# Kernel optimization log

Measured on AMD Instinct MI355X. Metric: run time of the kernel, lower is better.

Reference implementation:

```python
import jax, jax.numpy as jnp
import numpy as np

N = 50000
E = 800000
IN_DIM = 256
HID = 64
HEADS = 6
OUT_DIM = 32
NEG_SLOPE = 0.2


def gat_conv(x, src, dst, W, att_src, att_dst, bias, heads, ch, n_nodes):
    """PyG GATConv (eval mode): lin proj, per-edge LeakyReLU attention,
    segment softmax over destination neighborhoods, scatter-add aggregate.
    src/dst already include self-loops. Returns [n_nodes, heads, ch]."""
    h = (x @ W).reshape(n_nodes, heads, ch)            # [N,H,C]
    a_src = jnp.sum(h * att_src, axis=-1)              # [N,H]
    a_dst = jnp.sum(h * att_dst, axis=-1)              # [N,H]
    e = jax.nn.leaky_relu(a_src[src] + a_dst[dst], NEG_SLOPE)   # [E,H]
    m = jax.ops.segment_max(e, dst, num_segments=n_nodes)       # [N,H]
    ex = jnp.exp(e - m[dst])                                    # [E,H]
    denom = jax.ops.segment_sum(ex, dst, num_segments=n_nodes)  # [N,H]
    alpha = ex / denom[dst]                                     # [E,H]
    out = jax.ops.segment_sum(h[src] * alpha[:, :, None], dst, num_segments=n_nodes)
    return out + bias.reshape(1, heads, ch)


def setup_inputs() -> dict:
    key = jax.random.key(0)
    ks = jax.random.split(key, 10)
    x = jax.random.normal(ks[0], (N, IN_DIM), dtype=jnp.float32)
    edge_index = jax.random.randint(ks[1], (2, E), 0, N, dtype=jnp.int64)
    s1 = 1.0 / np.sqrt(IN_DIM)
    W1 = jax.random.normal(ks[2], (IN_DIM, HEADS * HID), dtype=jnp.float32) * s1
    att_src1 = jax.random.normal(ks[3], (1, HEADS, HID), dtype=jnp.float32) * 0.1
    att_dst1 = jax.random.normal(ks[4], (1, HEADS, HID), dtype=jnp.float32) * 0.1
    b1 = jnp.zeros((HEADS * HID,), dtype=jnp.float32)
    s2 = 1.0 / np.sqrt(HEADS * HID)
    W2 = jax.random.normal(ks[5], (HEADS * HID, OUT_DIM), dtype=jnp.float32) * s2
    att_src2 = jax.random.normal(ks[6], (1, 1, OUT_DIM), dtype=jnp.float32) * 0.1
    att_dst2 = jax.random.normal(ks[7], (1, 1, OUT_DIM), dtype=jnp.float32) * 0.1
    b2 = jnp.zeros((OUT_DIM,), dtype=jnp.float32)
    return {"x": x, "edge_index": edge_index, "W1": W1, "att_src1": att_src1,
            "att_dst1": att_dst1, "b1": b1, "W2": W2, "att_src2": att_src2,
            "att_dst2": att_dst2, "b2": b2}


def reference(x, edge_index, W1, att_src1, att_dst1, b1, W2, att_src2, att_dst2, b2):
    # PyG GATConv default add_self_loops=True
    loops = jnp.arange(N, dtype=edge_index.dtype)
    src = jnp.concatenate([edge_index[0], loops])
    dst = jnp.concatenate([edge_index[1], loops])
    h1 = gat_conv(x, src, dst, W1, att_src1, att_dst1, b1, HEADS, HID, N)
    h1 = jax.nn.relu(h1.reshape(N, HEADS * HID))  # concat=True, then ReLU; dropout = identity (eval)
    h2 = gat_conv(h1, src, dst, W2, att_src2, att_dst2, b2, 1, OUT_DIM, N)
    return h2.reshape(N, OUT_DIM)  # concat=False with 1 head == mean == squeeze
```

## Files before the change

kernel.cpp:

```cpp
#include <hip/hip_runtime.h>
#include <hip/hip_bf16.h>

#define NN 50000
#define EE 800000
#define IN_DIM 256
#define HID 64
#define HEADS 6
#define D1 384
#define OUT_DIM 32
#define NEG_SLOPE 0.2f
#define CAP 128
#define NBLK 196

typedef unsigned int uint32;
typedef unsigned short ushort_t;
typedef short short8 __attribute__((ext_vector_type(8)));
typedef float f32x4 __attribute__((ext_vector_type(4)));
typedef ushort_t ushort8 __attribute__((ext_vector_type(8)));

__device__ __forceinline__ ushort_t f2bf(float f) {
    uint32 u = __builtin_bit_cast(uint32, f);
    u += 0x7fffu + ((u >> 16) & 1u);
    return (ushort_t)(u >> 16);
}
__device__ __forceinline__ float bf2f(ushort_t s) {
    uint32 u = ((uint32)s) << 16;
    return __builtin_bit_cast(float, u);
}
__device__ __forceinline__ float lo16(uint32 d) { return __builtin_bit_cast(float, d << 16); }
__device__ __forceinline__ float hi16(uint32 d) { return __builtin_bit_cast(float, d & 0xffff0000u); }


__global__ void hist_kernel(const int* __restrict__ dst, int* __restrict__ deg) {
    int i = blockIdx.x * 256 + threadIdx.x;
    if (i < EE) atomicAdd(&deg[dst[i]], 1);
}

__global__ __launch_bounds__(256) void scan1_kernel(const int* __restrict__ deg,
                                                    int* __restrict__ blockSums) {
    int t = threadIdx.x;
    int i = blockIdx.x * 256 + t;
    int v = (i < NN) ? (deg[i] + 1) : 0;
#pragma unroll
    for (int o = 32; o; o >>= 1) v += __shfl_xor(v, o);
    __shared__ int ws[4];
    if ((t & 63) == 0) ws[t >> 6] = v;
    __syncthreads();
    if (t == 0) blockSums[blockIdx.x] = ws[0] + ws[1] + ws[2] + ws[3];
}

__global__ __launch_bounds__(256) void scan2_kernel(const int* __restrict__ blockSums,
                                                    int* __restrict__ blockPrefix,
                                                    int* __restrict__ offsets) {
    int t = threadIdx.x;
    int lane = t & 63, w = t >> 6;
    int v = (t < NBLK) ? blockSums[t] : 0;
    int x = v;
#pragma unroll
    for (int o = 1; o < 64; o <<= 1) {
        int y = __shfl_up(x, o);
        if (lane >= o) x += y;
    }
    __shared__ int ws[4];
    if (lane == 63) ws[w] = x;
    __syncthreads();
    int wpre = 0;
#pragma unroll
    for (int k = 0; k < 4; ++k) if (k < w) wpre += ws[k];
    int incl = x + wpre;
    if (t < NBLK) blockPrefix[t] = incl - v;
    if (t == NBLK - 1) offsets[NN] = incl;
}

__global__ __launch_bounds__(256) void scan3_kernel(const int* __restrict__ deg,
                                                    const int* __restrict__ blockPrefix,
                                                    int* __restrict__ offsets,
                                                    int* __restrict__ cursor) {
    int t = threadIdx.x;
    int i = blockIdx.x * 256 + t;
    int lane = t & 63, w = t >> 6;
    int v = (i < NN) ? (deg[i] + 1) : 0;
    int x = v;
#pragma unroll
    for (int o = 1; o < 64; o <<= 1) {
        int y = __shfl_up(x, o);
        if (lane >= o) x += y;
    }
    __shared__ int ws[4];
    if (lane == 63) ws[w] = x;
    __syncthreads();
    int wpre = 0;
#pragma unroll
    for (int k = 0; k < 4; ++k) if (k < w) wpre += ws[k];
    int excl = x + wpre - v + blockPrefix[blockIdx.x];
    if (i < NN) { offsets[i] = excl; cursor[i] = excl; }
}

__global__ void scatter_kernel(const int* __restrict__ src, const int* __restrict__ dst,
                               int* __restrict__ cursor, int* __restrict__ srcIdx) {
    int i = blockIdx.x * 256 + threadIdx.x;
    if (i >= EE + NN) return;
    int s, d;
    if (i < EE) { s = src[i]; d = dst[i]; }
    else        { s = i - EE; d = s; }
    int pos = atomicAdd(&cursor[d], 1);
    srcIdx[pos] = s;
}


__global__ __launch_bounds__(256) void w1t_kernel(const float* __restrict__ W1,
                                                  ushort_t* __restrict__ W1Tb) {
    __shared__ float tile[32][33];
    int tx = threadIdx.x & 31, ty = threadIdx.x >> 5;
    int n0 = blockIdx.x * 32;
    int k0 = blockIdx.y * 32;
#pragma unroll
    for (int i = 0; i < 4; ++i)
        tile[ty + i * 8][tx] = W1[(k0 + ty + i * 8) * D1 + n0 + tx];
    __syncthreads();
#pragma unroll
    for (int i = 0; i < 4; ++i)
        W1Tb[(n0 + ty + i * 8) * IN_DIM + k0 + tx] = f2bf(tile[tx][ty + i * 8]);
}

__global__ __launch_bounds__(256) void w2t_kernel(const float* __restrict__ W2,
                                                  ushort_t* __restrict__ W2Tb) {
    int idx = blockIdx.x * 256 + threadIdx.x;
    if (idx < D1 * OUT_DIM) {
        int k = idx >> 5, n = idx & 31;
        W2Tb[n * D1 + k] = f2bf(W2[idx]);
    }
}


#define G1_BM 64
#define G1_BK 64

__global__ __launch_bounds__(256) void gemm1_kernel(const float* __restrict__ A,
                                                    const ushort_t* __restrict__ Bt,
                                                    const float* __restrict__ att_src,
                                                    const float* __restrict__ att_dst,
                                                    ushort_t* __restrict__ Cb,
                                                    float* __restrict__ a_src1,
                                                    float* __restrict__ a_dst1) {
    __shared__ __align__(16) ushort_t As[G1_BM][G1_BK];
    __shared__ __align__(16) ushort_t Bs[D1][G1_BK];
    __shared__ float redS[G1_BM][8];
    __shared__ float redD[G1_BM][8];
    int t = threadIdx.x;
    int m0 = blockIdx.x * G1_BM;
    int wid = t >> 6, lane = t & 63;
    int lrow = lane & 15, lk = lane >> 4;
    f32x4 acc[4][6] = {};
    for (int k0 = 0; k0 < IN_DIM; k0 += G1_BK) {
        {
            int r = t >> 3, c = t & 7;
#pragma unroll
            for (int p = 0; p < 2; ++p) {
                int row = p * 32 + r;
                int gr = m0 + row;
                float4 v0 = make_float4(0.f, 0.f, 0.f, 0.f), v1 = v0;
                if (gr < NN) {
                    const float* g = &A[(size_t)gr * IN_DIM + k0 + c * 8];
                    v0 = *reinterpret_cast<const float4*>(g);
                    v1 = *reinterpret_cast<const float4*>(g + 4);
                }
                ushort8 u;
                u[0] = f2bf(v0.x); u[1] = f2bf(v0.y); u[2] = f2bf(v0.z); u[3] = f2bf(v0.w);
                u[4] = f2bf(v1.x); u[5] = f2bf(v1.y); u[6] = f2bf(v1.z); u[7] = f2bf(v1.w);
                *reinterpret_cast<ushort8*>(&As[row][(c ^ (row & 7)) * 8]) = u;
            }
        }
        {
            int r = t >> 3, c = t & 7;
#pragma unroll
            for (int p = 0; p < 12; ++p) {
                int row = p * 32 + r;
                ushort8 u = *reinterpret_cast<const ushort8*>(&Bt[row * IN_DIM + k0 + c * 8]);
                *reinterpret_cast<ushort8*>(&Bs[row][(c ^ (row & 7)) * 8]) = u;
            }
        }
        __syncthreads();
#pragma unroll
        for (int kk = 0; kk < G1_BK; kk += 32) {
            int ckb = (kk >> 3) + lk;
            short8 af[4];
#pragma unroll
            for (int fm = 0; fm < 4; ++fm) {
                int m = fm * 16 + lrow;
                af[fm] = *reinterpret_cast<const short8*>(&As[m][(ckb ^ (m & 7)) * 8]);
            }
#pragma unroll
            for (int fn = 0; fn < 6; ++fn) {
                int n = wid * 96 + fn * 16 + lrow;
                short8 bfv = *reinterpret_cast<const short8*>(&Bs[n][(ckb ^ (n & 7)) * 8]);
#pragma unroll
                for (int fm = 0; fm < 4; ++fm)
                    acc[fm][fn] = __builtin_amdgcn_mfma_f32_16x16x32_bf16(af[fm], bfv, acc[fm][fn], 0, 0, 0);
            }
        }
        __syncthreads();
    }
    float atS[6], atD[6];
#pragma unroll
    for (int fn = 0; fn < 6; ++fn) {
        int col = wid * 96 + fn * 16 + lrow;
        atS[fn] = att_src[col];
        atD[fn] = att_dst[col];
    }
    int split = (wid & 1) ? 2 : 4;
#pragma unroll
    for (int fm = 0; fm < 4; ++fm) {
#pragma unroll
        for (int r = 0; r < 4; ++r) {
            int rowl = fm * 16 + lk * 4 + r;
            int row = m0 + rowl;
            float vsA = 0.f, vsB = 0.f, vdA = 0.f, vdB = 0.f;
#pragma unroll
            for (int fn = 0; fn < 6; ++fn) {
                float v = acc[fm][fn][r];
                if (fn < split) { vsA += v * atS[fn]; vdA += v * atD[fn]; }
                else            { vsB += v * atS[fn]; vdB += v * atD[fn]; }
            }
#pragma unroll
            for (int o = 8; o; o >>= 1) {
                vsA += __shfl_xor(vsA, o); vsB += __shfl_xor(vsB, o);
                vdA += __shfl_xor(vdA, o); vdB += __shfl_xor(vdB, o);
            }
            if (lrow == 0) {
                redS[rowl][wid * 2 + 0] = vsA; redS[rowl][wid * 2 + 1] = vsB;
                redD[rowl][wid * 2 + 0] = vdA; redD[rowl][wid * 2 + 1] = vdB;
            }
            if (row < NN) {
#pragma unroll
                for (int fn = 0; fn < 6; ++fn) {
                    int col = wid * 96 + fn * 16 + lrow;
                    Cb[(size_t)row * D1 + col] = f2bf(acc[fm][fn][r]);
                }
            }
        }
    }
    __syncthreads();
    if (t < G1_BM) {
        int row = m0 + t;
        if (row < NN) {
            float s0 = redS[t][0], s1 = redS[t][1] + redS[t][2], s2 = redS[t][3];
            float s3 = redS[t][4], s4 = redS[t][5] + redS[t][6], s5 = redS[t][7];
            float d0 = redD[t][0], d1 = redD[t][1] + redD[t][2], d2 = redD[t][3];
            float d3 = redD[t][4], d4 = redD[t][5] + redD[t][6], d5 = redD[t][7];
            float* ps = &a_src1[(size_t)row * HEADS];
            float* pd = &a_dst1[(size_t)row * HEADS];
            ps[0] = s0; ps[1] = s1; ps[2] = s2; ps[3] = s3; ps[4] = s4; ps[5] = s5;
            pd[0] = d0; pd[1] = d1; pd[2] = d2; pd[3] = d3; pd[4] = d4; pd[5] = d5;
        }
    }
}


__global__ __launch_bounds__(256, 4) void agg1_kernel(const uint32* __restrict__ H1d,
                                                      const float* __restrict__ a_src,
                                                      const float* __restrict__ a_dst,
                                                      const int* __restrict__ offsets,
                                                      const int* __restrict__ srcIdx,
                                                      const float* __restrict__ b1,
                                                      uint32* __restrict__ out1d) {
    __shared__ float pl[4][HEADS][CAP + 1];
    __shared__ int   sl[4][CAP];
    int w = threadIdx.x >> 6, lane = threadIdx.x & 63;
    int hb = lane >> 5;
    int n = blockIdx.x * 4 + w;
    const float2* asv = (const float2*)a_src;
    float ad[HEADS];
#pragma unroll
    for (int h = 0; h < HEADS; ++h) ad[h] = a_dst[n * HEADS + h];
    float ldn[HEADS] = {0.f, 0.f, 0.f, 0.f, 0.f, 0.f};
    float acc[6] = {0.f, 0.f, 0.f, 0.f, 0.f, 0.f};
    int beg = offsets[n], end = offsets[n + 1];
    for (int cbeg = beg; cbeg < end; cbeg += CAP) {
        int L = end - cbeg; if (L > CAP) L = CAP;
        for (int tI = lane; tI < L; tI += 64) {
            int s = srcIdx[cbeg + tI];
            sl[w][tI] = s;
            float2 e0 = asv[s * 3 + 0];
            float2 e1 = asv[s * 3 + 1];
            float2 e2 = asv[s * 3 + 2];
            float ev[6] = {e0.x, e0.y, e1.x, e1.y, e2.x, e2.y};
#pragma unroll
            for (int h = 0; h < HEADS; ++h) {
                float e = ev[h] + ad[h];
                e = e > 0.f ? e : NEG_SLOPE * e;
                float p = __expf(e);
                pl[w][h][tI] = p;
                ldn[h] += p;
            }
        }
        int j = 0;
        for (; j + 4 <= L; j += 4) {
            int s0 = sl[w][j], s1 = sl[w][j + 1], s2 = sl[w][j + 2], s3 = sl[w][j + 3];
            const uint32* h0 = H1d + (size_t)s0 * 192 + lane;
            const uint32* h1 = H1d + (size_t)s1 * 192 + lane;
            const uint32* h2 = H1d + (size_t)s2 * 192 + lane;
            const uint32* h3 = H1d + (size_t)s3 * 192 + lane;
            uint32 a0 = h0[0], a1 = h0[64], a2 = h0[128];
            uint32 b0 = h1[0], b1v_ = h1[64], b2 = h1[128];
            uint32 c0 = h2[0], c1 = h2[64], c2 = h2[128];
            uint32 d0 = h3[0], d1 = h3[64], d2 = h3[128];
            float p00 = pl[w][hb][j],     p01 = pl[w][2 + hb][j],     p02 = pl[w][4 + hb][j];
            float p10 = pl[w][hb][j + 1], p11 = pl[w][2 + hb][j + 1], p12 = pl[w][4 + hb][j + 1];
            float p20 = pl[w][hb][j + 2], p21 = pl[w][2 + hb][j + 2], p22 = pl[w][4 + hb][j + 2];
            float p30 = pl[w][hb][j + 3], p31 = pl[w][2 + hb][j + 3], p32 = pl[w][4 + hb][j + 3];
            acc[0] += p00 * lo16(a0); acc[1] += p00 * hi16(a0);
            acc[2] += p01 * lo16(a1); acc[3] += p01 * hi16(a1);
            acc[4] += p02 * lo16(a2); acc[5] += p02 * hi16(a2);
            acc[0] += p10 * lo16(b0); acc[1] += p10 * hi16(b0);
            acc[2] += p11 * lo16(b1v_); acc[3] += p11 * hi16(b1v_);
            acc[4] += p12 * lo16(b2); acc[5] += p12 * hi16(b2);
            acc[0] += p20 * lo16(c0); acc[1] += p20 * hi16(c0);
            acc[2] += p21 * lo16(c1); acc[3] += p21 * hi16(c1);
            acc[4] += p22 * lo16(c2); acc[5] += p22 * hi16(c2);
            acc[0] += p30 * lo16(d0); acc[1] += p30 * hi16(d0);
            acc[2] += p31 * lo16(d1); acc[3] += p31 * hi16(d1);
            acc[4] += p32 * lo16(d2); acc[5] += p32 * hi16(d2);
        }
        for (; j < L; ++j) {
            int s0 = sl[w][j];
            const uint32* h0 = H1d + (size_t)s0 * 192 + lane;
            uint32 x0 = h0[0], x1 = h0[64], x2 = h0[128];
            float p0 = pl[w][hb][j], p1 = pl[w][2 + hb][j], p2 = pl[w][4 + hb][j];
            acc[0] += p0 * lo16(x0); acc[1] += p0 * hi16(x0);
            acc[2] += p1 * lo16(x1); acc[3] += p1 * hi16(x1);
            acc[4] += p2 * lo16(x2); acc[5] += p2 * hi16(x2);
        }
    }
#pragma unroll
    for (int h = 0; h < HEADS; ++h) {
#pragma unroll
        for (int o = 32; o; o >>= 1) ldn[h] += __shfl_xor(ldn[h], o);
    }
    float dsel[3];
#pragma unroll
    for (int k = 0; k < 3; ++k) dsel[k] = hb ? ldn[2 * k + 1] : ldn[2 * k];
    const float2* b1v = (const float2*)b1;
#pragma unroll
    for (int k = 0; k < 3; ++k) {
        float2 bb = b1v[k * 64 + lane];
        float v0 = fmaxf(acc[2 * k]     / dsel[k] + bb.x, 0.f);
        float v1 = fmaxf(acc[2 * k + 1] / dsel[k] + bb.y, 0.f);
        out1d[(size_t)n * 192 + k * 64 + lane] = (uint32)f2bf(v0) | ((uint32)f2bf(v1) << 16);
    }
}


#define G2_ROWS 256

__global__ __launch_bounds__(256) void gemm2_kernel(const ushort_t* __restrict__ Xb,
                                                    const ushort_t* __restrict__ W2Tb,
                                                    const float* __restrict__ att_src2,
                                                    const float* __restrict__ att_dst2,
                                                    ushort_t* __restrict__ H2b,
                                                    float* __restrict__ a_src2,
                                                    float* __restrict__ a_dst2) {
    __shared__ __align__(16) ushort_t Ws[OUT_DIM][D1];
    __shared__ __align__(16) ushort_t Xs[G2_ROWS][64];
    int t = threadIdx.x;
    int wid = t >> 6, lane = t & 63;
    int lrow = lane & 15, lk = lane >> 4;
    int m0 = blockIdx.x * G2_ROWS;
#pragma unroll
    for (int p = 0; p < 6; ++p) {
        int chunk = p * 256 + t;
        int nr = chunk / 48, c = chunk % 48;
        ushort8 u = *reinterpret_cast<const ushort8*>(&W2Tb[nr * D1 + c * 8]);
        int span = c >> 3, cc = c & 7;
        *reinterpret_cast<ushort8*>(&Ws[nr][(cc ^ (nr & 7)) * 8 + span * 64]) = u;
    }
    f32x4 acc[4][2] = {};
    for (int kc = 0; kc < 6; ++kc) {
        int k0 = kc * 64;
        {
            int r = t >> 3, c = t & 7;
#pragma unroll
            for (int p = 0; p < 8; ++p) {
                int row = p * 32 + r;
                int gr = m0 + row;
                ushort8 u = {0, 0, 0, 0, 0, 0, 0, 0};
                if (gr < NN) u = *reinterpret_cast<const ushort8*>(&Xb[(size_t)gr * D1 + k0 + c * 8]);
                *reinterpret_cast<ushort8*>(&Xs[row][(c ^ (row & 7)) * 8]) = u;
            }
        }
        __syncthreads();
#pragma unroll
        for (int kk = 0; kk < 64; kk += 32) {
            int ckb = (kk >> 3) + lk;
            short8 af[4];
#pragma unroll
            for (int fm = 0; fm < 4; ++fm) {
                int mm = wid * 64 + fm * 16 + lrow;
                af[fm] = *reinterpret_cast<const short8*>(&Xs[mm][(ckb ^ (mm & 7)) * 8]);
            }
#pragma unroll
            for (int fn = 0; fn < 2; ++fn) {
                int nn2 = fn * 16 + lrow;
                short8 bfv = *reinterpret_cast<const short8*>(&Ws[nn2][(ckb ^ (nn2 & 7)) * 8 + kc * 64]);
#pragma unroll
                for (int fm = 0; fm < 4; ++fm)
                    acc[fm][fn] = __builtin_amdgcn_mfma_f32_16x16x32_bf16(af[fm], bfv, acc[fm][fn], 0, 0, 0);
            }
        }
        __syncthreads();
    }
    float as2a = att_src2[lrow], as2b = att_src2[16 + lrow];
    float ad2a = att_dst2[lrow], ad2b = att_dst2[16 + lrow];
#pragma unroll
    for (int fm = 0; fm < 4; ++fm) {
#pragma unroll
        for (int r = 0; r < 4; ++r) {
            int row = m0 + wid * 64 + fm * 16 + lk * 4 + r;
            float h0 = acc[fm][0][r], h1 = acc[fm][1][r];
            float vs = h0 * as2a + h1 * as2b;
            float vd = h0 * ad2a + h1 * ad2b;
#pragma unroll
            for (int o = 8; o; o >>= 1) {
                vs += __shfl_xor(vs, o);
                vd += __shfl_xor(vd, o);
            }
            if (row < NN) {
                H2b[(size_t)row * OUT_DIM + lrow]      = f2bf(h0);
                H2b[(size_t)row * OUT_DIM + 16 + lrow] = f2bf(h1);
                if (lrow == 0) { a_src2[row] = vs; a_dst2[row] = vd; }
            }
        }
    }
}


__global__ __launch_bounds__(256, 4) void agg2_kernel(const ushort_t* __restrict__ H2b,
                                                      const float* __restrict__ a_src,
                                                      const float* __restrict__ a_dst,
                                                      const int* __restrict__ offsets,
                                                      const int* __restrict__ srcIdx,
                                                      const float* __restrict__ b2,
                                                      float* __restrict__ out) {
    __shared__ float pl[4][CAP];
    __shared__ int   sl[4][CAP];
    int w = threadIdx.x >> 6, lane = threadIdx.x & 63;
    int n = blockIdx.x * 4 + w;
    int q = lane & 15, par = lane >> 4;
    const uint32* H2d = (const uint32*)H2b;
    float ad = a_dst[n];
    float ldn = 0.f, ax = 0.f, ay = 0.f;
    int beg = offsets[n], end = offsets[n + 1];
    for (int cbeg = beg; cbeg < end; cbeg += CAP) {
        int L = end - cbeg; if (L > CAP) L = CAP;
        for (int tI = lane; tI < L; tI += 64) {
            int s = srcIdx[cbeg + tI];
            sl[w][tI] = s;
            float e = a_src[s] + ad;
            e = e > 0.f ? e : NEG_SLOPE * e;
            float p = __expf(e);
            pl[w][tI] = p;
            ldn += p;
        }
        int j = 0;
        for (; j + 8 <= L; j += 8) {
            int s0 = sl[w][j + par], s1 = sl[w][j + 4 + par];
            float p0 = pl[w][j + par], p1 = pl[w][j + 4 + par];
            uint32 d0 = H2d[(size_t)s0 * 16 + q];
            uint32 d1 = H2d[(size_t)s1 * 16 + q];
            ax += p0 * lo16(d0) + p1 * lo16(d1);
            ay += p0 * hi16(d0) + p1 * hi16(d1);
        }
        for (; j < L; j += 4) {
            int jj = j + par;
            if (jj < L) {
                int s = sl[w][jj];
                float p = pl[w][jj];
                uint32 d = H2d[(size_t)s * 16 + q];
                ax += p * lo16(d);
                ay += p * hi16(d);
            }
        }
    }
#pragma unroll
    for (int o = 32; o; o >>= 1) ldn += __shfl_xor(ldn, o);
    ax += __shfl_xor(ax, 16); ax += __shfl_xor(ax, 32);
    ay += __shfl_xor(ay, 16); ay += __shfl_xor(ay, 32);
    if (lane < 16) {
        float2 bb = ((const float2*)b2)[q];
        float2 o;
        o.x = ax / ldn + bb.x;
        o.y = ay / ldn + bb.y;
        ((float2*)out)[(size_t)n * 16 + q] = o;
    }
}


static inline size_t align256(size_t x) { return (x + 255) & ~size_t(255); }

extern "C" void kernel_launch(void* const* d_in, const int* in_sizes, int n_in,
                              void* d_out, int out_size, void* d_ws, size_t ws_size,
                              hipStream_t stream) {
    const float* x        = (const float*)d_in[0];
    const int*   ei       = (const int*)d_in[1];
    const float* W1       = (const float*)d_in[2];
    const float* att_src1 = (const float*)d_in[3];
    const float* att_dst1 = (const float*)d_in[4];
    const float* b1       = (const float*)d_in[5];
    const float* W2       = (const float*)d_in[6];
    const float* att_src2 = (const float*)d_in[7];
    const float* att_dst2 = (const float*)d_in[8];
    const float* b2       = (const float*)d_in[9];
    float* out = (float*)d_out;

    const int* e_src = ei;
    const int* e_dst = ei + EE;

    char* p = (char*)d_ws;
    ushort_t* H1b   = (ushort_t*)p; p += align256(sizeof(ushort_t) * (size_t)NN * D1);
    ushort_t* OUT1b = (ushort_t*)p; p += align256(sizeof(ushort_t) * (size_t)NN * D1);
    ushort_t* H2b   = (ushort_t*)p; p += align256(sizeof(ushort_t) * (size_t)NN * OUT_DIM);
    ushort_t* W1Tb  = (ushort_t*)p; p += align256(sizeof(ushort_t) * D1 * IN_DIM);
    ushort_t* W2Tb  = (ushort_t*)p; p += align256(sizeof(ushort_t) * D1 * OUT_DIM);
    float* AS1  = (float*)p; p += align256(sizeof(float) * NN * HEADS);
    float* AD1  = (float*)p; p += align256(sizeof(float) * NN * HEADS);
    float* AS2  = (float*)p; p += align256(sizeof(float) * NN);
    float* AD2  = (float*)p; p += align256(sizeof(float) * NN);
    int*   DEG  = (int*)p;   p += align256(sizeof(int) * NN);
    int*   OFF  = (int*)p;   p += align256(sizeof(int) * (NN + 1));
    int*   CUR  = (int*)p;   p += align256(sizeof(int) * NN);
    int*   BSUM = (int*)p;   p += align256(sizeof(int) * NBLK);
    int*   BPRE = (int*)p;   p += align256(sizeof(int) * NBLK);
    int*   SIDX = (int*)p;   p += align256(sizeof(int) * (EE + NN));

    hipMemsetAsync(DEG, 0, sizeof(int) * NN, stream);
    w1t_kernel<<<dim3(D1 / 32, IN_DIM / 32), 256, 0, stream>>>(W1, W1Tb);
    w2t_kernel<<<48, 256, 0, stream>>>(W2, W2Tb);
    hist_kernel<<<(EE + 255) / 256, 256, 0, stream>>>(e_dst, DEG);
    scan1_kernel<<<NBLK, 256, 0, stream>>>(DEG, BSUM);
    scan2_kernel<<<1, 256, 0, stream>>>(BSUM, BPRE, OFF);
    scan3_kernel<<<NBLK, 256, 0, stream>>>(DEG, BPRE, OFF, CUR);
    scatter_kernel<<<(EE + NN + 255) / 256, 256, 0, stream>>>(e_src, e_dst, CUR, SIDX);

    gemm1_kernel<<<(NN + G1_BM - 1) / G1_BM, 256, 0, stream>>>(x, W1Tb, att_src1, att_dst1, H1b, AS1, AD1);
    agg1_kernel<<<NN / 4, 256, 0, stream>>>((const uint32*)H1b, AS1, AD1, OFF, SIDX, b1, (uint32*)OUT1b);

    gemm2_kernel<<<(NN + G2_ROWS - 1) / G2_ROWS, 256, 0, stream>>>(OUT1b, W2Tb, att_src2, att_dst2, H2b, AS2, AD2);
    agg2_kernel<<<NN / 4, 256, 0, stream>>>(H2b, AS2, AD2, OFF, SIDX, b2, out);
}
```

Baseline: 328.7 us.

## Stage full A tile in LDS, read W1 fragments from global, nontemporal stores

The first GEMM now loads the whole 64x256 bf16 activation tile into shared memory once, with a single barrier. The transposed W1 fragments are read straight from global memory (where they should stay L2-resident) instead of being staged in LDS each k-step, which removes the per-k-step barriers and the large B shared buffer. That raises occupancy, but the MFMA loop now waits on global-load latency. The aggregation outputs use nontemporal stores so they do not pollute the cache.

```diff
diff --git a/kernel.cpp b/kernel.cpp
--- a/kernel.cpp
+++ b/kernel.cpp
@@ -16,6 +16,7 @@
 typedef unsigned short ushort_t;
 typedef short short8 __attribute__((ext_vector_type(8)));
 typedef float f32x4 __attribute__((ext_vector_type(4)));
+typedef float f32x2 __attribute__((ext_vector_type(2)));
 typedef ushort_t ushort8 __attribute__((ext_vector_type(8)));
 
 __device__ __forceinline__ ushort_t f2bf(float f) {
@@ -134,7 +135,6 @@
 
 
 #define G1_BM 64
-#define G1_BK 64
 
 __global__ __launch_bounds__(256) void gemm1_kernel(const float* __restrict__ A,
                                                     const ushort_t* __restrict__ Bt,
@@ -143,63 +143,50 @@
                                                     ushort_t* __restrict__ Cb,
                                                     float* __restrict__ a_src1,
                                                     float* __restrict__ a_dst1) {
-    __shared__ __align__(16) ushort_t As[G1_BM][G1_BK];
-    __shared__ __align__(16) ushort_t Bs[D1][G1_BK];
+    __shared__ __align__(16) ushort_t As[G1_BM][IN_DIM];
     __shared__ float redS[G1_BM][8];
     __shared__ float redD[G1_BM][8];
     int t = threadIdx.x;
     int m0 = blockIdx.x * G1_BM;
     int wid = t >> 6, lane = t & 63;
     int lrow = lane & 15, lk = lane >> 4;
+    {
+        int r = t >> 2, cq = (t & 3) * 8;
+        int gr = m0 + r;
+#pragma unroll
+        for (int p = 0; p < 8; ++p) {
+            int c = cq + p;
+            float4 v0 = make_float4(0.f, 0.f, 0.f, 0.f), v1 = v0;
+            if (gr < NN) {
+                const float* g = &A[(size_t)gr * IN_DIM + c * 8];
+                v0 = *reinterpret_cast<const float4*>(g);
+                v1 = *reinterpret_cast<const float4*>(g + 4);
+            }
+            ushort8 u;
+            u[0] = f2bf(v0.x); u[1] = f2bf(v0.y); u[2] = f2bf(v0.z); u[3] = f2bf(v0.w);
+            u[4] = f2bf(v1.x); u[5] = f2bf(v1.y); u[6] = f2bf(v1.z); u[7] = f2bf(v1.w);
+            *reinterpret_cast<ushort8*>(&As[r][(c ^ (r & 7)) * 8]) = u;
+        }
+    }
+    __syncthreads();
     f32x4 acc[4][6] = {};
-    for (int k0 = 0; k0 < IN_DIM; k0 += G1_BK) {
-        {
-            int r = t >> 3, c = t & 7;
-#pragma unroll
-            for (int p = 0; p < 2; ++p) {
-                int row = p * 32 + r;
-                int gr = m0 + row;
-                float4 v0 = make_float4(0.f, 0.f, 0.f, 0.f), v1 = v0;
-                if (gr < NN) {
-                    const float* g = &A[(size_t)gr * IN_DIM + k0 + c * 8];
-                    v0 = *reinterpret_cast<const float4*>(g);
-                    v1 = *reinterpret_cast<const float4*>(g + 4);
-                }
-                ushort8 u;
-                u[0] = f2bf(v0.x); u[1] = f2bf(v0.y); u[2] = f2bf(v0.z); u[3] = f2bf(v0.w);
-                u[4] = f2bf(v1.x); u[5] = f2bf(v1.y); u[6] = f2bf(v1.z); u[7] = f2bf(v1.w);
-                *reinterpret_cast<ushort8*>(&As[row][(c ^ (row & 7)) * 8]) = u;
-            }
-        }
-        {
-            int r = t >> 3, c = t & 7;
-#pragma unroll
-            for (int p = 0; p < 12; ++p) {
-                int row = p * 32 + r;
-                ushort8 u = *reinterpret_cast<const ushort8*>(&Bt[row * IN_DIM + k0 + c * 8]);
-                *reinterpret_cast<ushort8*>(&Bs[row][(c ^ (row & 7)) * 8]) = u;
-            }
-        }
-        __syncthreads();
-#pragma unroll
-        for (int kk = 0; kk < G1_BK; kk += 32) {
-            int ckb = (kk >> 3) + lk;
-            short8 af[4];
-#pragma unroll
-            for (int fm = 0; fm < 4; ++fm) {
-                int m = fm * 16 + lrow;
-                af[fm] = *reinterpret_cast<const short8*>(&As[m][(ckb ^ (m & 7)) * 8]);
-            }
-#pragma unroll
-            for (int fn = 0; fn < 6; ++fn) {
-                int n = wid * 96 + fn * 16 + lrow;
-                short8 bfv = *reinterpret_cast<const short8*>(&Bs[n][(ckb ^ (n & 7)) * 8]);
-#pragma unroll
-                for (int fm = 0; fm < 4; ++fm)
-                    acc[fm][fn] = __builtin_amdgcn_mfma_f32_16x16x32_bf16(af[fm], bfv, acc[fm][fn], 0, 0, 0);
-            }
-        }
-        __syncthreads();
+#pragma unroll
+    for (int kk = 0; kk < IN_DIM; kk += 32) {
+        int ckb = (kk >> 3) + lk;
+        short8 af[4];
+#pragma unroll
+        for (int fm = 0; fm < 4; ++fm) {
+            int m = fm * 16 + lrow;
+            af[fm] = *reinterpret_cast<const short8*>(&As[m][(ckb ^ (m & 7)) * 8]);
+        }
+#pragma unroll
+        for (int fn = 0; fn < 6; ++fn) {
+            int n = wid * 96 + fn * 16 + lrow;
+            short8 bfv = *reinterpret_cast<const short8*>(&Bt[n * IN_DIM + kk + lk * 8]);
+#pragma unroll
+            for (int fm = 0; fm < 4; ++fm)
+                acc[fm][fn] = __builtin_amdgcn_mfma_f32_16x16x32_bf16(af[fm], bfv, acc[fm][fn], 0, 0, 0);
+        }
     }
     float atS[6], atD[6];
 #pragma unroll
@@ -346,7 +333,8 @@
         float2 bb = b1v[k * 64 + lane];
         float v0 = fmaxf(acc[2 * k]     / dsel[k] + bb.x, 0.f);
         float v1 = fmaxf(acc[2 * k + 1] / dsel[k] + bb.y, 0.f);
-        out1d[(size_t)n * 192 + k * 64 + lane] = (uint32)f2bf(v0) | ((uint32)f2bf(v1) << 16);
+        uint32 pk = (uint32)f2bf(v0) | ((uint32)f2bf(v1) << 16);
+        __builtin_nontemporal_store(pk, &out1d[(size_t)n * 192 + k * 64 + lane]);
     }
 }
 
@@ -487,10 +475,10 @@
     ay += __shfl_xor(ay, 16); ay += __shfl_xor(ay, 32);
     if (lane < 16) {
         float2 bb = ((const float2*)b2)[q];
-        float2 o;
-        o.x = ax / ldn + bb.x;
-        o.y = ay / ldn + bb.y;
-        ((float2*)out)[(size_t)n * 16 + q] = o;
+        f32x2 o;
+        o[0] = ax / ldn + bb.x;
+        o[1] = ay / ldn + bb.y;
+        __builtin_nontemporal_store(o, (f32x2*)&out[(size_t)n * 32 + q * 2]);
     }
 }
 
@@ -532,7 +520,7 @@
     int*   BPRE = (int*)p;   p += align256(sizeof(int) * NBLK);
     int*   SIDX = (int*)p;   p += align256(sizeof(int) * (EE + NN));
 
-    hipMemsetAsync(DEG, 0, sizeof(int) * NN, stream);
+    (void)hipMemsetAsync(DEG, 0, sizeof(int) * NN, stream);
     w1t_kernel<<<dim3(D1 / 32, IN_DIM / 32), 256, 0, stream>>>(W1, W1Tb);
     w2t_kernel<<<48, 256, 0, stream>>>(W2, W2Tb);
     hist_kernel<<<(EE + 255) / 256, 256, 0, stream>>>(e_dst, DEG);
```

Result: no change. 334.6 us (+1.8%).
